# Performance work log

Hardware: AMD Instinct MI355X
Metric: run time of the kernel (lower is better)

The kernel has to match this reference:

```python
import jax, jax.numpy as jnp
import numpy as np

D_MODEL = 1024
D_FF = 4096
NUM_EXPERTS = 8
TOP_K = 2  # expert_capacity


def setup_inputs() -> dict:
    key = jax.random.key(0)
    ks = jax.random.split(key, 7)
    s_in = 1.0 / np.sqrt(D_MODEL)
    s_ff = 1.0 / np.sqrt(D_FF)
    x = jax.random.normal(ks[0], (2, 2048, D_MODEL), dtype=jnp.float32)
    gate_w = jax.random.uniform(ks[1], (NUM_EXPERTS, D_MODEL), jnp.float32, -s_in, s_in)
    gate_b = jax.random.uniform(ks[2], (NUM_EXPERTS,), jnp.float32, -s_in, s_in)
    w1 = jax.random.uniform(ks[3], (NUM_EXPERTS, D_MODEL, D_FF), jnp.float32, -s_in, s_in)
    b1 = jax.random.uniform(ks[4], (NUM_EXPERTS, D_FF), jnp.float32, -s_in, s_in)
    w2 = jax.random.uniform(ks[5], (NUM_EXPERTS, D_FF, D_MODEL), jnp.float32, -s_ff, s_ff)
    b2 = jax.random.uniform(ks[6], (NUM_EXPERTS, D_MODEL), jnp.float32, -s_ff, s_ff)
    return {"x": x, "gate_w": gate_w, "gate_b": gate_b,
            "w1": w1, "b1": b1, "w2": w2, "b2": b2}


def reference(x, gate_w, gate_b, w1, b1, w2, b2):
    E = gate_w.shape[0]
    # Router
    logits = jnp.einsum('bsd,ed->bse', x, gate_w) + gate_b  # [B,S,E]
    top_vals, top_idx = jax.lax.top_k(logits, TOP_K)        # [B,S,K]
    top_w = jax.nn.softmax(top_vals, axis=-1)               # softmax over the top-k logits
    probs = jax.nn.softmax(logits, axis=-1)
    usage = probs.mean(axis=(0, 1))                         # [E]
    load_balancing_loss = E * jnp.sum(usage ** 2) - 1.0
    # Combine weights: sum over top-k slots of weight * one_hot(expert)
    combine = jnp.sum(top_w[..., None] * jax.nn.one_hot(top_idx, E, dtype=x.dtype), axis=2)  # [B,S,E]
    # All experts over all tokens (faithful to the naive dense-then-mask module)
    h = jax.nn.gelu(jnp.einsum('bsd,edf->ebsf', x, w1) + b1[:, None, None, :], approximate=False)
    expert_out = jnp.einsum('ebsf,efd->ebsd', h, w2) + b2[:, None, None, :]  # [E,B,S,D]
    output = jnp.einsum('bse,ebsd->bsd', combine, expert_out)
    return output, load_balancing_loss
```

## Files before the change

### kernel.cpp

```cpp
#include <hip/hip_runtime.h>
#include <hip/hip_bf16.h>
#include <math.h>


#define D_MODEL 1024
#define D_FF    4096
#define NE      8
#define NTOK    4096
#define CAP     4096

typedef __attribute__((ext_vector_type(4))) float f32x4;
typedef __attribute__((ext_vector_type(8))) short s16x8;

__device__ __forceinline__ short f2bf(float f) {
    union { float f; unsigned u; } v; v.f = f;
    unsigned r = v.u + 0x7FFFu + ((v.u >> 16) & 1u);
    return (short)(r >> 16);
}

__device__ __forceinline__ void gload16(const void* g, void* l) {
    __builtin_amdgcn_global_load_lds(
        (const __attribute__((address_space(1))) unsigned*)g,
        (__attribute__((address_space(3))) unsigned*)l, 16, 0, 0);
}

__global__ __launch_bounds__(256) void router_kernel(
    const float* __restrict__ x, const float* __restrict__ gw,
    const float* __restrict__ gb,
    float* __restrict__ usage, int* __restrict__ eidx, float* __restrict__ wgt)
{
    __shared__ float s_gw[NE][D_MODEL];
    __shared__ float s_usage[NE];
    int tid = threadIdx.x;
    for (int i = tid * 4; i < NE * D_MODEL; i += 256 * 4)
        *(f32x4*)&s_gw[0][i] = *(const f32x4*)(gw + i);
    if (tid < NE) s_usage[tid] = 0.f;
    __syncthreads();

    int wid = tid >> 6, lane = tid & 63;
    int wave_stride = gridDim.x * 4;
    float l_usage[NE];
#pragma unroll
    for (int e = 0; e < NE; e++) l_usage[e] = 0.f;

    for (int t = blockIdx.x * 4 + wid; t < NTOK; t += wave_stride) {
        const float* xr = x + (size_t)t * D_MODEL;
        float acc[NE];
#pragma unroll
        for (int e = 0; e < NE; e++) acc[e] = 0.f;
        for (int i = lane * 4; i < D_MODEL; i += 64 * 4) {
            f32x4 xv = *(const f32x4*)(xr + i);
#pragma unroll
            for (int e = 0; e < NE; e++) {
                f32x4 gv = *(const f32x4*)&s_gw[e][i];
                acc[e] += xv[0]*gv[0] + xv[1]*gv[1] + xv[2]*gv[2] + xv[3]*gv[3];
            }
        }
#pragma unroll
        for (int e = 0; e < NE; e++) {
            float a = acc[e];
            for (int off = 32; off; off >>= 1) a += __shfl_down(a, off);
            acc[e] = a;
        }
        if (lane == 0) {
            float logits[NE];
            float mx = -1e30f;
#pragma unroll
            for (int e = 0; e < NE; e++) { logits[e] = acc[e] + gb[e]; mx = fmaxf(mx, logits[e]); }
            float se = 0.f;
            float pe[NE];
#pragma unroll
            for (int e = 0; e < NE; e++) { pe[e] = expf(logits[e] - mx); se += pe[e]; }
            float inv = 1.f / se;
#pragma unroll
            for (int e = 0; e < NE; e++) l_usage[e] += pe[e] * inv;
            int i0 = 0;
#pragma unroll
            for (int e = 1; e < NE; e++) if (logits[e] > logits[i0]) i0 = e;
            int i1 = -1;
#pragma unroll
            for (int e = 0; e < NE; e++) {
                if (e == i0) continue;
                if (i1 < 0 || logits[e] > logits[i1]) i1 = e;
            }
            float w0 = 1.f / (1.f + expf(logits[i1] - logits[i0]));
            eidx[t] = i0 | (i1 << 8);
            wgt[t] = w0;
        }
    }
    if (lane == 0) {
#pragma unroll
        for (int e = 0; e < NE; e++) atomicAdd(&s_usage[e], l_usage[e]);
    }
    __syncthreads();
    if (tid < NE) atomicAdd(&usage[tid], s_usage[tid]);
}

__global__ __launch_bounds__(256) void build_lists(
    const int* __restrict__ eidx, const float* __restrict__ wgt,
    int* __restrict__ cnt, int* __restrict__ tok_list, float* __restrict__ wt_list)
{
    int e = blockIdx.x;
    __shared__ int s_cnt;
    if (threadIdx.x == 0) s_cnt = 0;
    __syncthreads();
    for (int t = threadIdx.x; t < NTOK; t += 256) {
        int p = eidx[t];
        float w0 = wgt[t];
        if ((p & 255) == e) {
            int s = atomicAdd(&s_cnt, 1);
            tok_list[e * CAP + s] = t; wt_list[e * CAP + s] = w0;
        }
        if ((p >> 8) == e) {
            int s = atomicAdd(&s_cnt, 1);
            tok_list[e * CAP + s] = t; wt_list[e * CAP + s] = 1.f - w0;
        }
    }
    __syncthreads();
    if (threadIdx.x == 0) cnt[e] = s_cnt;
}

__global__ void compute_offsets(const int* __restrict__ cnt, int* __restrict__ offsets)
{
    int o = 0;
    for (int e = 0; e < NE; e++) { offsets[e] = o; o += cnt[e]; }
}

__global__ void write_loss(const float* __restrict__ usage, float* __restrict__ out_loss)
{
    float s = 0.f;
    for (int e = 0; e < NE; e++) { float u = usage[e] / (float)NTOK; s += u * u; }
    *out_loss = (float)NE * s - 1.f;
}

__global__ __launch_bounds__(256) void cvt_x_kernel(
    const float* __restrict__ x, short* __restrict__ xb)
{
    int i = (blockIdx.x * 256 + threadIdx.x) * 8;
    f32x4 a = *(const f32x4*)(x + i);
    f32x4 b = *(const f32x4*)(x + i + 4);
    s16x8 r;
    r[0]=f2bf(a[0]); r[1]=f2bf(a[1]); r[2]=f2bf(a[2]); r[3]=f2bf(a[3]);
    r[4]=f2bf(b[0]); r[5]=f2bf(b[1]); r[6]=f2bf(b[2]); r[7]=f2bf(b[3]);
    *(s16x8*)(xb + i) = r;
}

__global__ __launch_bounds__(256) void transpose_cvt(
    const float* __restrict__ src, short* __restrict__ dst, int R, int C)
{
    __shared__ float tile[64][65];
    int e = blockIdx.z;
    src += (size_t)e * R * C;
    dst += (size_t)e * R * C;
    int c0 = blockIdx.x * 64, r0 = blockIdx.y * 64;
    int tid = threadIdx.x;
    int lr = tid >> 2, lc = (tid & 3) * 16;

    const float* s = src + (size_t)(r0 + lr) * C + c0 + lc;
#pragma unroll
    for (int j = 0; j < 4; j++)
        *(f32x4*)&tile[lr][lc + j * 4] = *(const f32x4*)(s + j * 4);
    __syncthreads();

    short* d = dst + (size_t)(c0 + lr) * R + r0 + lc;
    s16x8 v0, v1;
#pragma unroll
    for (int j = 0; j < 8; j++) v0[j] = f2bf(tile[lc + j][lr]);
#pragma unroll
    for (int j = 0; j < 8; j++) v1[j] = f2bf(tile[lc + 8 + j][lr]);
    *(s16x8*)d = v0;
    *(s16x8*)(d + 8) = v1;
}

__global__ __launch_bounds__(256) void gemm1_kernel(
    const short* __restrict__ XB, const short* __restrict__ W1T,
    const float* __restrict__ b1, const int* __restrict__ cnt,
    const int* __restrict__ offsets, const int* __restrict__ tok_list,
    short* __restrict__ H)
{
    int e  = blockIdx.y >> 5;
    int tm = blockIdx.y & 31;
    int ce = cnt[e];
    if (tm * 128 >= ce) return;
    int n0 = blockIdx.x * 128;

    __shared__ __align__(16) short As[128][32];
    __shared__ __align__(16) short Bs[128][32];

    int tid = threadIdx.x;
    int lane = tid & 63, wid = tid >> 6;
    int wr = wid >> 1, wc = wid & 1;
    int lrow = lane & 15, kgr = lane >> 4;

    int srow = wid * 16 + (lane >> 2);
    int scol = (lane & 3) * 8;
    int am0 = tm * 128 + srow, am1 = am0 + 64;
    int tok0 = tok_list[e * CAP + (am0 < ce ? am0 : 0)];
    int tok1 = tok_list[e * CAP + (am1 < ce ? am1 : 0)];
    const short* asrc0 = XB + (size_t)tok0 * D_MODEL + scol;
    const short* asrc1 = XB + (size_t)tok1 * D_MODEL + scol;
    const short* bsrc0 = W1T + ((size_t)e * D_FF + n0 + srow) * D_MODEL + scol;
    const short* bsrc1 = bsrc0 + (size_t)64 * D_MODEL;

    f32x4 acc[4][4] = {};
    for (int kt = 0; kt < D_MODEL; kt += 32) {
        gload16(asrc0 + kt, &As[wid * 16][0]);
        gload16(asrc1 + kt, &As[64 + wid * 16][0]);
        gload16(bsrc0 + kt, &Bs[wid * 16][0]);
        gload16(bsrc1 + kt, &Bs[64 + wid * 16][0]);
        __syncthreads();

        s16x8 a[4], b[4];
#pragma unroll
        for (int i = 0; i < 4; i++) {
            a[i] = *(const s16x8*)&As[wr * 64 + i * 16 + lrow][kgr * 8];
            b[i] = *(const s16x8*)&Bs[wc * 64 + i * 16 + lrow][kgr * 8];
        }
#pragma unroll
        for (int i = 0; i < 4; i++)
#pragma unroll
        for (int j = 0; j < 4; j++)
            acc[i][j] = __builtin_amdgcn_mfma_f32_16x16x32_bf16(a[i], b[j], acc[i][j], 0, 0, 0);
        __syncthreads();
    }

    int offe = offsets[e];
    float bn[4];
#pragma unroll
    for (int j = 0; j < 4; j++) bn[j] = b1[e * D_FF + n0 + wc * 64 + j * 16 + lrow];
#pragma unroll
    for (int i = 0; i < 4; i++) {
#pragma unroll
        for (int q = 0; q < 4; q++) {
            int m = tm * 128 + wr * 64 + i * 16 + kgr * 4 + q;
            if (m >= ce) continue;
            short* hrow = H + (size_t)(offe + m) * D_FF;
#pragma unroll
            for (int j = 0; j < 4; j++) {
                int n = n0 + wc * 64 + j * 16 + lrow;
                float v = acc[i][j][q] + bn[j];
                v = 0.5f * v * (1.f + erff(v * 0.70710678118654752f));
                hrow[n] = f2bf(v);
            }
        }
    }
}

__global__ __launch_bounds__(256) void gemm2_kernel(
    const short* __restrict__ H, const short* __restrict__ W2T,
    const float* __restrict__ b2, const int* __restrict__ cnt,
    const int* __restrict__ offsets, const int* __restrict__ tok_list,
    const float* __restrict__ wt_list, float* __restrict__ out)
{
    int e  = blockIdx.y >> 5;
    int tm = blockIdx.y & 31;
    int ce = cnt[e];
    if (tm * 128 >= ce) return;
    int offe = offsets[e];
    int n0 = blockIdx.x * 128;

    __shared__ __align__(16) short As[128][32];
    __shared__ __align__(16) short Bs[128][32];

    int tid = threadIdx.x;
    int lane = tid & 63, wid = tid >> 6;
    int wr = wid >> 1, wc = wid & 1;
    int lrow = lane & 15, kgr = lane >> 4;

    int srow = wid * 16 + (lane >> 2);
    int scol = (lane & 3) * 8;
    int am0 = tm * 128 + srow, am1 = am0 + 64;
    const short* asrc0 = H + (size_t)(offe + (am0 < ce ? am0 : 0)) * D_FF + scol;
    const short* asrc1 = H + (size_t)(offe + (am1 < ce ? am1 : 0)) * D_FF + scol;
    const short* bsrc0 = W2T + ((size_t)e * D_MODEL + n0 + srow) * D_FF + scol;
    const short* bsrc1 = bsrc0 + (size_t)64 * D_FF;

    f32x4 acc[4][4] = {};
    for (int kt = 0; kt < D_FF; kt += 32) {
        gload16(asrc0 + kt, &As[wid * 16][0]);
        gload16(asrc1 + kt, &As[64 + wid * 16][0]);
        gload16(bsrc0 + kt, &Bs[wid * 16][0]);
        gload16(bsrc1 + kt, &Bs[64 + wid * 16][0]);
        __syncthreads();

        s16x8 a[4], b[4];
#pragma unroll
        for (int i = 0; i < 4; i++) {
            a[i] = *(const s16x8*)&As[wr * 64 + i * 16 + lrow][kgr * 8];
            b[i] = *(const s16x8*)&Bs[wc * 64 + i * 16 + lrow][kgr * 8];
        }
#pragma unroll
        for (int i = 0; i < 4; i++)
#pragma unroll
        for (int j = 0; j < 4; j++)
            acc[i][j] = __builtin_amdgcn_mfma_f32_16x16x32_bf16(a[i], b[j], acc[i][j], 0, 0, 0);
        __syncthreads();
    }

    float bn[4];
#pragma unroll
    for (int j = 0; j < 4; j++) bn[j] = b2[e * D_MODEL + n0 + wc * 64 + j * 16 + lrow];
#pragma unroll
    for (int i = 0; i < 4; i++) {
#pragma unroll
        for (int q = 0; q < 4; q++) {
            int m = tm * 128 + wr * 64 + i * 16 + kgr * 4 + q;
            if (m >= ce) continue;
            int tokm = tok_list[e * CAP + m];
            float wt = wt_list[e * CAP + m];
            float* orow = out + (size_t)tokm * D_MODEL;
#pragma unroll
            for (int j = 0; j < 4; j++) {
                int n = n0 + wc * 64 + j * 16 + lrow;
                atomicAdd(&orow[n], wt * (acc[i][j][q] + bn[j]));
            }
        }
    }
}

extern "C" void kernel_launch(void* const* d_in, const int* in_sizes, int n_in,
                              void* d_out, int out_size, void* d_ws, size_t ws_size,
                              hipStream_t stream)
{
    const float* x  = (const float*)d_in[0];
    const float* gw = (const float*)d_in[1];
    const float* gb = (const float*)d_in[2];
    const float* w1 = (const float*)d_in[3];
    const float* b1 = (const float*)d_in[4];
    const float* w2 = (const float*)d_in[5];
    const float* b2 = (const float*)d_in[6];
    float* out = (float*)d_out;

    char* w = (char*)d_ws;
    int*   cnt      = (int*)(w + 0);
    float* usage    = (float*)(w + 32);
    int*   offsets  = (int*)(w + 64);
    int*   tok_list = (int*)(w + 128);
    float* wt_list  = (float*)(w + 128 + NE * CAP * 4);
    short* WT       = (short*)(w + 128 + 2 * NE * CAP * 4);
    short* H        = (short*)((char*)WT + (size_t)NE * D_FF * D_MODEL * 2);
    int*   eidx     = (int*)WT;
    float* wgt      = (float*)(WT + NTOK * 2);
    short* XB       = (short*)d_out;

    hipMemsetAsync(d_ws, 0, 128, stream);

    router_kernel<<<256, 256, 0, stream>>>(x, gw, gb, usage, eidx, wgt);
    build_lists<<<NE, 256, 0, stream>>>(eidx, wgt, cnt, tok_list, wt_list);
    compute_offsets<<<1, 1, 0, stream>>>(cnt, offsets);
    cvt_x_kernel<<<NTOK * D_MODEL / (256 * 8), 256, 0, stream>>>(x, XB);

    transpose_cvt<<<dim3(D_FF / 64, D_MODEL / 64, NE), 256, 0, stream>>>(w1, WT, D_MODEL, D_FF);
    gemm1_kernel<<<dim3(D_FF / 128, NE * (CAP / 128)), 256, 0, stream>>>(
        XB, WT, b1, cnt, offsets, tok_list, H);

    hipMemsetAsync(d_out, 0, (size_t)out_size * sizeof(float), stream);
    write_loss<<<1, 1, 0, stream>>>(usage, out + (size_t)NTOK * D_MODEL);

    transpose_cvt<<<dim3(D_MODEL / 64, D_FF / 64, NE), 256, 0, stream>>>(w2, WT, D_FF, D_MODEL);
    gemm2_kernel<<<dim3(D_MODEL / 128, NE * (CAP / 128)), 256, 0, stream>>>(
        H, WT, b2, cnt, offsets, tok_list, wt_list, out);
}
```

Before: 366.7 us.

## Double-buffer LDS in expert GEMMs, swizzle LDS columns, split-K gemm2

Both expert GEMMs now use double-buffered LDS tiles, issuing the next k-tile's async global-to-LDS loads before computing the current one and synchronising with explicit vmcnt waits and barriers instead of two __syncthreads per step. LDS columns are XOR-swizzled on both the store and read side to reduce bank conflicts. gemm2 is split along K into two halves via a z grid dimension, adding only one bias, which doubles its block count for better occupancy at the cost of twice as many atomic adds to the output.

Measured after the change: 389.9 us. 1.06x slower.

```diff
diff --git a/kernel.cpp b/kernel.cpp
--- a/kernel.cpp
+++ b/kernel.cpp
@@ -172,6 +172,29 @@
     *(s16x8*)(d + 8) = v1;
 }
 
+#define GEMM_STAGE(AS, BS, BUF, KT)                          \
+    gload16(asrc0 + (KT), &AS[BUF][wid * 16][0]);            \
+    gload16(asrc1 + (KT), &AS[BUF][64 + wid * 16][0]);       \
+    gload16(bsrc0 + (KT), &BS[BUF][wid * 16][0]);            \
+    gload16(bsrc1 + (KT), &BS[BUF][64 + wid * 16][0]);
+
+#define GEMM_COMPUTE(AS, BS, BUF)                                              \
+    {                                                                          \
+        s16x8 a[4], b[4];                                                      \
+        int cidx = (kgr ^ ((lrow >> 1) & 3)) * 8;                              \
+        _Pragma("unroll")                                                      \
+        for (int i = 0; i < 4; i++) {                                          \
+            a[i] = *(const s16x8*)&AS[BUF][wr * 64 + i * 16 + lrow][cidx];     \
+            b[i] = *(const s16x8*)&BS[BUF][wc * 64 + i * 16 + lrow][cidx];     \
+        }                                                                      \
+        _Pragma("unroll")                                                      \
+        for (int i = 0; i < 4; i++)                                            \
+            _Pragma("unroll")                                                  \
+            for (int j = 0; j < 4; j++)                                        \
+                acc[i][j] = __builtin_amdgcn_mfma_f32_16x16x32_bf16(           \
+                    a[i], b[j], acc[i][j], 0, 0, 0);                           \
+    }
+
 __global__ __launch_bounds__(256) void gemm1_kernel(
     const short* __restrict__ XB, const short* __restrict__ W1T,
     const float* __restrict__ b1, const int* __restrict__ cnt,
@@ -184,8 +207,8 @@
     if (tm * 128 >= ce) return;
     int n0 = blockIdx.x * 128;
 
-    __shared__ __align__(16) short As[128][32];
-    __shared__ __align__(16) short Bs[128][32];
+    __shared__ __align__(16) short As[2][128][32];
+    __shared__ __align__(16) short Bs[2][128][32];
 
     int tid = threadIdx.x;
     int lane = tid & 63, wid = tid >> 6;
@@ -193,7 +216,7 @@
     int lrow = lane & 15, kgr = lane >> 4;
 
     int srow = wid * 16 + (lane >> 2);
-    int scol = (lane & 3) * 8;
+    int scol = ((lane & 3) ^ ((lane >> 3) & 3)) * 8;
     int am0 = tm * 128 + srow, am1 = am0 + 64;
     int tok0 = tok_list[e * CAP + (am0 < ce ? am0 : 0)];
     int tok1 = tok_list[e * CAP + (am1 < ce ? am1 : 0)];
@@ -203,26 +226,19 @@
     const short* bsrc1 = bsrc0 + (size_t)64 * D_MODEL;
 
     f32x4 acc[4][4] = {};
-    for (int kt = 0; kt < D_MODEL; kt += 32) {
-        gload16(asrc0 + kt, &As[wid * 16][0]);
-        gload16(asrc1 + kt, &As[64 + wid * 16][0]);
-        gload16(bsrc0 + kt, &Bs[wid * 16][0]);
-        gload16(bsrc1 + kt, &Bs[64 + wid * 16][0]);
-        __syncthreads();
-
-        s16x8 a[4], b[4];
-#pragma unroll
-        for (int i = 0; i < 4; i++) {
-            a[i] = *(const s16x8*)&As[wr * 64 + i * 16 + lrow][kgr * 8];
-            b[i] = *(const s16x8*)&Bs[wc * 64 + i * 16 + lrow][kgr * 8];
-        }
-#pragma unroll
-        for (int i = 0; i < 4; i++)
-#pragma unroll
-        for (int j = 0; j < 4; j++)
-            acc[i][j] = __builtin_amdgcn_mfma_f32_16x16x32_bf16(a[i], b[j], acc[i][j], 0, 0, 0);
-        __syncthreads();
-    }
+    GEMM_STAGE(As, Bs, 0, 0);
+    int cur = 0;
+    for (int kt = 32; kt < D_MODEL; kt += 32) {
+        GEMM_STAGE(As, Bs, cur ^ 1, kt);
+        asm volatile("s_waitcnt vmcnt(4)" ::: "memory");
+        __builtin_amdgcn_s_barrier();
+        GEMM_COMPUTE(As, Bs, cur);
+        __builtin_amdgcn_s_barrier();
+        cur ^= 1;
+    }
+    asm volatile("s_waitcnt vmcnt(0)" ::: "memory");
+    __builtin_amdgcn_s_barrier();
+    GEMM_COMPUTE(As, Bs, cur);
 
     int offe = offsets[e];
     float bn[4];
@@ -258,9 +274,12 @@
     if (tm * 128 >= ce) return;
     int offe = offsets[e];
     int n0 = blockIdx.x * 128;
-
-    __shared__ __align__(16) short As[128][32];
-    __shared__ __align__(16) short Bs[128][32];
+    int kz = blockIdx.z;
+    const int KSPAN = D_FF / 2;
+    int kbase = kz * KSPAN;
+
+    __shared__ __align__(16) short As[2][128][32];
+    __shared__ __align__(16) short Bs[2][128][32];
 
     int tid = threadIdx.x;
     int lane = tid & 63, wid = tid >> 6;
@@ -268,38 +287,32 @@
     int lrow = lane & 15, kgr = lane >> 4;
 
     int srow = wid * 16 + (lane >> 2);
-    int scol = (lane & 3) * 8;
+    int scol = ((lane & 3) ^ ((lane >> 3) & 3)) * 8;
     int am0 = tm * 128 + srow, am1 = am0 + 64;
-    const short* asrc0 = H + (size_t)(offe + (am0 < ce ? am0 : 0)) * D_FF + scol;
-    const short* asrc1 = H + (size_t)(offe + (am1 < ce ? am1 : 0)) * D_FF + scol;
-    const short* bsrc0 = W2T + ((size_t)e * D_MODEL + n0 + srow) * D_FF + scol;
+    const short* asrc0 = H + (size_t)(offe + (am0 < ce ? am0 : 0)) * D_FF + kbase + scol;
+    const short* asrc1 = H + (size_t)(offe + (am1 < ce ? am1 : 0)) * D_FF + kbase + scol;
+    const short* bsrc0 = W2T + ((size_t)e * D_MODEL + n0 + srow) * D_FF + kbase + scol;
     const short* bsrc1 = bsrc0 + (size_t)64 * D_FF;
 
     f32x4 acc[4][4] = {};
-    for (int kt = 0; kt < D_FF; kt += 32) {
-        gload16(asrc0 + kt, &As[wid * 16][0]);
-        gload16(asrc1 + kt, &As[64 + wid * 16][0]);
-        gload16(bsrc0 + kt, &Bs[wid * 16][0]);
-        gload16(bsrc1 + kt, &Bs[64 + wid * 16][0]);
-        __syncthreads();
-
-        s16x8 a[4], b[4];
-#pragma unroll
-        for (int i = 0; i < 4; i++) {
-            a[i] = *(const s16x8*)&As[wr * 64 + i * 16 + lrow][kgr * 8];
-            b[i] = *(const s16x8*)&Bs[wc * 64 + i * 16 + lrow][kgr * 8];
-        }
-#pragma unroll
-        for (int i = 0; i < 4; i++)
-#pragma unroll
-        for (int j = 0; j < 4; j++)
-            acc[i][j] = __builtin_amdgcn_mfma_f32_16x16x32_bf16(a[i], b[j], acc[i][j], 0, 0, 0);
-        __syncthreads();
-    }
+    GEMM_STAGE(As, Bs, 0, 0);
+    int cur = 0;
+    for (int kt = 32; kt < KSPAN; kt += 32) {
+        GEMM_STAGE(As, Bs, cur ^ 1, kt);
+        asm volatile("s_waitcnt vmcnt(4)" ::: "memory");
+        __builtin_amdgcn_s_barrier();
+        GEMM_COMPUTE(As, Bs, cur);
+        __builtin_amdgcn_s_barrier();
+        cur ^= 1;
+    }
+    asm volatile("s_waitcnt vmcnt(0)" ::: "memory");
+    __builtin_amdgcn_s_barrier();
+    GEMM_COMPUTE(As, Bs, cur);
 
     float bn[4];
 #pragma unroll
-    for (int j = 0; j < 4; j++) bn[j] = b2[e * D_MODEL + n0 + wc * 64 + j * 16 + lrow];
+    for (int j = 0; j < 4; j++)
+        bn[j] = (kz == 0) ? b2[e * D_MODEL + n0 + wc * 64 + j * 16 + lrow] : 0.f;
 #pragma unroll
     for (int i = 0; i < 4; i++) {
 #pragma unroll
@@ -358,6 +371,6 @@
     write_loss<<<1, 1, 0, stream>>>(usage, out + (size_t)NTOK * D_MODEL);
 
     transpose_cvt<<<dim3(D_MODEL / 64, D_FF / 64, NE), 256, 0, stream>>>(w2, WT, D_FF, D_MODEL);
-    gemm2_kernel<<<dim3(D_MODEL / 128, NE * (CAP / 128)), 256, 0, stream>>>(
+    gemm2_kernel<<<dim3(D_MODEL / 128, NE * (CAP / 128), 2), 256, 0, stream>>>(
         H, WT, b2, cnt, offsets, tok_list, wt_list, out);
 }
```
